# Kernel optimization log

Measured on AMD Instinct MI355X. Metric: run time of the kernel, lower is better.

## Reference

```python
import jax, jax.numpy as jnp
import numpy as np

NUM_HEADS = 16  # matches init_kwargs


def _linear(x, W, b):
    # torch nn.Linear: x @ W.T + b
    return jnp.matmul(x, W.T) + b


def setup_inputs() -> dict:
    key = jax.random.key(0)
    ks = jax.random.split(key, 5)
    B, S, Dm = 8, 2048, 1024
    scale = 0.02
    return {
        "q": jax.random.normal(ks[0], (B, S, Dm), dtype=jnp.float32),
        "k": jax.random.normal(ks[1], (B, S, Dm), dtype=jnp.float32),
        "v": jax.random.normal(ks[2], (B, S, Dm), dtype=jnp.float32),
        "W": jax.random.normal(ks[3], (Dm, Dm), dtype=jnp.float32) * scale,
        "b": jax.random.normal(ks[4], (Dm,), dtype=jnp.float32) * scale,
    }


def reference(q, k, v, W, b):
    B, S, Dm = q.shape
    H = NUM_HEADS
    D = Dm // H  # head_dim

    def proj(x):
        # linear -> view(B, S, H, D) -> transpose(2, 3): (B, S, D, H)
        # NOTE: original code transposes dims 2 and 3 (head_dim <-> heads),
        # NOT the usual (1, 2); we reproduce that exactly.
        y = _linear(x, W, b).reshape(B, S, H, D)
        return jnp.swapaxes(y, 2, 3)  # (B, S, D, H)

    qh, kh, vh = proj(q), proj(k), proj(v)

    # scores: (B, S, D, H) @ (B, S, H, D) -> (B, S, D, D), scaled by sqrt(head_dim)
    logits = jnp.einsum("bsdh,bseh->bsde", qh, kh) / jnp.sqrt(jnp.float32(D))
    attn = jax.nn.softmax(logits, axis=-1)
    out = jnp.einsum("bsde,bseh->bsdh", attn, vh)  # (B, S, D, H)

    # transpose(1, 2) -> (B, D, S, H), then view(B, -1, model_dim)
    concat = jnp.swapaxes(out, 1, 2).reshape(B, -1, Dm)  # (B, S, Dm)
    return _linear(concat, W, b)
```

## Files before the change

### kernel.cpp

```cpp
#include <hip/hip_runtime.h>
#include <hip/hip_fp16.h>
#include <math.h>

typedef _Float16 f16;
typedef _Float16 half8_t __attribute__((ext_vector_type(8)));
typedef _Float16 half2_t __attribute__((ext_vector_type(2)));
typedef __fp16   fp16x2  __attribute__((ext_vector_type(2)));
typedef float    float4_t __attribute__((ext_vector_type(4)));

__device__ f16 Wh[1024 * 1024];

__device__ __forceinline__ void gl_lds16(const void* g, void* l) {
    __builtin_amdgcn_global_load_lds(
        (const __attribute__((address_space(1))) void*)g,
        (__attribute__((address_space(3))) void*)l,
        16, 0, 0);
}

__device__ __forceinline__ half2_t pkrtz(float a, float b) {
    fp16x2 r = __builtin_amdgcn_cvt_pkrtz(a, b);
    return __builtin_bit_cast(half2_t, r);
}

__device__ __forceinline__ float fdot2(half2_t a, half2_t b, float c) {
    return __builtin_amdgcn_fdot2(__builtin_bit_cast(fp16x2, a),
                                  __builtin_bit_cast(fp16x2, b), c, false);
}

__device__ __forceinline__ half8_t cvt8(float4_t lo, float4_t hi) {
    half2_t p0 = pkrtz(lo[0], lo[1]);
    half2_t p1 = pkrtz(lo[2], lo[3]);
    half2_t p2 = pkrtz(hi[0], hi[1]);
    half2_t p3 = pkrtz(hi[2], hi[3]);
    half8_t r;
    r[0] = p0[0]; r[1] = p0[1]; r[2] = p1[0]; r[3] = p1[1];
    r[4] = p2[0]; r[5] = p2[1]; r[6] = p3[0]; r[7] = p3[1];
    return r;
}

__global__ __launch_bounds__(256) void convert_w_kernel(const float* __restrict__ W) {
    const int i = (blockIdx.x * 256 + threadIdx.x) * 8;
    const float4_t a = *(const float4_t*)(W + i);
    const float4_t b = *(const float4_t*)(W + i + 4);
    half8_t h;
#pragma unroll
    for (int t = 0; t < 4; ++t) h[t] = (f16)a[t];
#pragma unroll
    for (int t = 0; t < 4; ++t) h[4 + t] = (f16)b[t];
    *(half8_t*)(Wh + i) = h;
}

template <typename TA, typename TC>
__device__ __forceinline__ void gemm_tile(
    const TA* __restrict__ A, const float* __restrict__ bias,
    TC* __restrict__ C)
{
    constexpr int K = 1024, N = 1024;
    constexpr bool AF32 = (sizeof(TA) == 4);
    __shared__ __align__(16) char smem[(AF32 ? 32768 : 16384) + 16384];
    float* Asf = (float*)smem;
    f16*   Ash = (f16*)smem;
    f16*   Bsh = (f16*)(smem + (AF32 ? 32768 : 16384));

    const int tid  = threadIdx.x;
    const int lane = tid & 63;
    const int wave = tid >> 6;
    const int wm = (wave >> 1) << 6;
    const int wn = (wave & 1) << 6;
    const int row0 = blockIdx.x * 128;
    const int col0 = blockIdx.y * 128;
    const int lrow = lane & 15;
    const int kq   = lane >> 4;

    float4_t acc[4][4];
#pragma unroll
    for (int i = 0; i < 4; ++i)
#pragma unroll
        for (int j = 0; j < 4; ++j)
            acc[i][j] = (float4_t){0.f, 0.f, 0.f, 0.f};

    for (int kt = 0; kt < K; kt += 64) {
#pragma unroll
        for (int it = 0; it < 4; ++it) {
            const int ch = tid + it * 256;
            const int r = ch >> 3, s = ch & 7;
            const f16* src = Wh + (size_t)(col0 + r) * K + kt + ((s ^ (r & 7)) << 3);
            gl_lds16(src, Bsh + ch * 8);
        }
        if constexpr (AF32) {
#pragma unroll
            for (int it = 0; it < 8; ++it) {
                const int ch = tid + it * 256;
                const int r = ch >> 4, s = ch & 15;
                const float* src = (const float*)A + (size_t)(row0 + r) * K + kt + ((s ^ (r & 15)) << 2);
                gl_lds16(src, Asf + ch * 4);
            }
        } else {
#pragma unroll
            for (int it = 0; it < 4; ++it) {
                const int ch = tid + it * 256;
                const int r = ch >> 3, s = ch & 7;
                const f16* src = (const f16*)A + (size_t)(row0 + r) * K + kt + ((s ^ (r & 7)) << 3);
                gl_lds16(src, Ash + ch * 8);
            }
        }
        __syncthreads();

#pragma unroll
        for (int ks = 0; ks < 2; ++ks) {
            half8_t af[4], bf[4];
#pragma unroll
            for (int i = 0; i < 4; ++i) {
                const int m = wm + i * 16 + lrow;
                if constexpr (AF32) {
                    const int c0 = ks * 8 + kq * 2;
                    const float4_t lo = *(const float4_t*)(Asf + m * 64 + ((c0 ^ (m & 15)) << 2));
                    const float4_t hi = *(const float4_t*)(Asf + m * 64 + (((c0 + 1) ^ (m & 15)) << 2));
                    af[i] = cvt8(lo, hi);
                } else {
                    af[i] = *(const half8_t*)(Ash + m * 64 + (((ks * 4 + kq) ^ (m & 7)) << 3));
                }
            }
#pragma unroll
            for (int j = 0; j < 4; ++j) {
                const int n = wn + j * 16 + lrow;
                bf[j] = *(const half8_t*)(Bsh + n * 64 + (((ks * 4 + kq) ^ (n & 7)) << 3));
            }
#pragma unroll
            for (int i = 0; i < 4; ++i)
#pragma unroll
                for (int j = 0; j < 4; ++j)
                    acc[i][j] = __builtin_amdgcn_mfma_f32_16x16x32_f16(af[i], bf[j], acc[i][j], 0, 0, 0);
        }
        __syncthreads();
    }

    const int ccol  = lane & 15;
    const int rbase = (lane >> 4) << 2;
#pragma unroll
    for (int j = 0; j < 4; ++j) {
        const int gcol = col0 + wn + j * 16 + ccol;
        const float bv = bias[gcol];
#pragma unroll
        for (int i = 0; i < 4; ++i) {
#pragma unroll
            for (int r = 0; r < 4; ++r) {
                const int grow = row0 + wm + i * 16 + rbase + r;
                C[(size_t)grow * N + gcol] = (TC)(acc[i][j][r] + bv);
            }
        }
    }
}

template <typename TA, typename TC>
__global__ __launch_bounds__(256) void gemm_kernel(
    const TA* __restrict__ A, const float* __restrict__ bias,
    TC* __restrict__ C)
{
    gemm_tile<TA, TC>(A, bias, C);
}

__global__ __launch_bounds__(256) void gemm_proj_kernel(
    const float* __restrict__ q, const float* __restrict__ k,
    const float* __restrict__ v, const float* __restrict__ bias,
    f16* __restrict__ cq, f16* __restrict__ ck, f16* __restrict__ cv)
{
    const int z = blockIdx.z;
    const float* A = (z == 0) ? q : (z == 1) ? k : v;
    f16*         C = (z == 0) ? cq : (z == 1) ? ck : cv;
    gemm_tile<float, f16>(A, bias, C);
}

__global__ __launch_bounds__(256) void attn_kernel(
    const f16* __restrict__ pq, const f16* __restrict__ pk,
    const f16* __restrict__ pv, f16* __restrict__ outp)
{
    __shared__ __align__(16) f16 Ks[4][64][24];
    __shared__ __align__(16) f16 Vs[4][16][72];
    const int lane = threadIdx.x & 63;
    const int wave = threadIdx.x >> 6;
    const int p = blockIdx.x * 4 + wave;
    const int b = p >> 11;
    const int s = p & 2047;
    const f16* qptr = pq + (size_t)p * 1024;
    const f16* kptr = pk + (size_t)p * 1024;
    const f16* vptr = pv + (size_t)p * 1024;

    {
        const int h  = lane >> 2;
        const int e0 = (lane & 3) << 4;
        const half8_t k0 = *(const half8_t*)(kptr + lane * 16);
        const half8_t k1 = *(const half8_t*)(kptr + lane * 16 + 8);
#pragma unroll
        for (int t = 0; t < 8; ++t) {
            Ks[wave][e0 + t][h]     = k0[t];
            Ks[wave][e0 + 8 + t][h] = k1[t];
        }
        const half8_t v0 = *(const half8_t*)(vptr + lane * 16);
        const half8_t v1 = *(const half8_t*)(vptr + lane * 16 + 8);
        *(half8_t*)&Vs[wave][h][e0]     = v0;
        *(half8_t*)&Vs[wave][h][e0 + 8] = v1;
    }
    half2_t qp2[8];
#pragma unroll
    for (int h2 = 0; h2 < 8; ++h2) {
        half2_t t;
        t[0] = qptr[(2 * h2) * 64 + lane];
        t[1] = qptr[(2 * h2 + 1) * 64 + lane];
        qp2[h2] = t;
    }
    __syncthreads();

    float a[64];
#pragma unroll
    for (int e = 0; e < 64; ++e) {
        const half8_t* kr = (const half8_t*)&Ks[wave][e][0];
        const half8_t ka = kr[0];
        const half8_t kb = kr[1];
        float acc = 0.f;
#pragma unroll
        for (int t = 0; t < 4; ++t) {
            half2_t k2a; k2a[0] = ka[2 * t]; k2a[1] = ka[2 * t + 1];
            half2_t k2b; k2b[0] = kb[2 * t]; k2b[1] = kb[2 * t + 1];
            acc = fdot2(qp2[t], k2a, acc);
            acc = fdot2(qp2[4 + t], k2b, acc);
        }
        a[e] = acc;
    }

    float m = a[0];
#pragma unroll
    for (int e = 1; e < 64; ++e) m = fmaxf(m, a[e]);
    float sum = 0.f;
#pragma unroll
    for (int e = 0; e < 64; ++e) {
        const float t = __expf((a[e] - m) * 0.125f);
        a[e] = t;
        sum += t;
    }
    const float inv = 1.f / sum;

    half2_t pk2[32];
#pragma unroll
    for (int e2 = 0; e2 < 32; ++e2)
        pk2[e2] = pkrtz(a[2 * e2], a[2 * e2 + 1]);

    float o[16];
#pragma unroll
    for (int h = 0; h < 16; ++h) {
        const half8_t* vr = (const half8_t*)&Vs[wave][h][0];
        float acc = 0.f;
#pragma unroll
        for (int q8 = 0; q8 < 8; ++q8) {
            const half8_t vv = vr[q8];
#pragma unroll
            for (int t = 0; t < 4; ++t) {
                half2_t v2; v2[0] = vv[2 * t]; v2[1] = vv[2 * t + 1];
                acc = fdot2(pk2[q8 * 4 + t], v2, acc);
            }
        }
        o[h] = acc;
    }

    half8_t o0, o1;
#pragma unroll
    for (int h = 0; h < 8; ++h) o0[h] = (f16)(o[h] * inv);
#pragma unroll
    for (int h = 0; h < 8; ++h) o1[h] = (f16)(o[8 + h] * inv);
    f16* dst = outp + ((size_t)(b * 64 + lane) * 2048 + s) * 16;
    *(half8_t*)dst       = o0;
    *(half8_t*)(dst + 8) = o1;
}

extern "C" void kernel_launch(void* const* d_in, const int* in_sizes, int n_in,
                              void* d_out, int out_size, void* d_ws, size_t ws_size,
                              hipStream_t stream)
{
    const float* q    = (const float*)d_in[0];
    const float* k    = (const float*)d_in[1];
    const float* v    = (const float*)d_in[2];
    const float* W    = (const float*)d_in[3];
    const float* bias = (const float*)d_in[4];
    float* out = (float*)d_out;

    const int M = 16384;
    const size_t elems = (size_t)M * 1024;

    f16* projq = (f16*)d_ws;
    f16* attn  = projq + elems;
    f16* projk = (f16*)d_out;
    f16* projv = projk + elems;

    convert_w_kernel<<<512, 256, 0, stream>>>(W);

    dim3 gridp(M / 128, 1024 / 128, 3);
    gemm_proj_kernel<<<gridp, 256, 0, stream>>>(q, k, v, bias, projq, projk, projv);
    attn_kernel<<<M / 4, 256, 0, stream>>>(projq, projk, projv, attn);
    dim3 grid(M / 128, 1024 / 128);
    gemm_kernel<f16, float><<<grid, 256, 0, stream>>>(attn, bias, out);
}
```

Baseline: 448.3 us.

## Use 256x256 double-buffered GEMM tiles with register-staged fp32 A conversion

```diff
diff --git a/kernel.cpp b/kernel.cpp
--- a/kernel.cpp
+++ b/kernel.cpp
@@ -50,102 +50,178 @@
     *(half8_t*)(Wh + i) = h;
 }
 
+
+__device__ __forceinline__ void stage16(const f16* __restrict__ base, f16* dst,
+                                        int tid, int kt) {
+#pragma unroll
+    for (int it = 0; it < 4; ++it) {
+        const int ch = tid + it * 512;
+        const int r = ch >> 3, s = ch & 7;
+        gl_lds16(base + (size_t)r * 1024 + kt + ((s ^ (r & 7)) << 3), dst + ch * 8);
+    }
+}
+
+__device__ __forceinline__ void loadA32(const float* __restrict__ base, int tid,
+                                        int kt, int itbase, float4_t g[4]) {
+#pragma unroll
+    for (int it = 0; it < 2; ++it) {
+        const int ch = tid + (itbase + it) * 512;
+        const int r = ch >> 3, s = ch & 7;
+        const float* p = base + (size_t)r * 1024 + kt + ((s ^ (r & 7)) << 3);
+        g[2 * it]     = *(const float4_t*)p;
+        g[2 * it + 1] = *(const float4_t*)(p + 4);
+    }
+}
+
+__device__ __forceinline__ void writeA32(f16* dst, int tid, int itbase,
+                                         const float4_t g[4]) {
+#pragma unroll
+    for (int it = 0; it < 2; ++it) {
+        const int ch = tid + (itbase + it) * 512;
+        *(half8_t*)(dst + ch * 8) = cvt8(g[2 * it], g[2 * it + 1]);
+    }
+}
+
 template <typename TA, typename TC>
-__device__ __forceinline__ void gemm_tile(
-    const TA* __restrict__ A, const float* __restrict__ bias,
-    TC* __restrict__ C)
-{
-    constexpr int K = 1024, N = 1024;
+__device__ __forceinline__ void gemm_tile256(const TA* __restrict__ A,
+                                             const float* __restrict__ bias,
+                                             TC* __restrict__ C) {
+    constexpr int K = 1024, N = 1024, NT = 16;
     constexpr bool AF32 = (sizeof(TA) == 4);
-    __shared__ __align__(16) char smem[(AF32 ? 32768 : 16384) + 16384];
-    float* Asf = (float*)smem;
-    f16*   Ash = (f16*)smem;
-    f16*   Bsh = (f16*)(smem + (AF32 ? 32768 : 16384));
+    __shared__ __align__(16) f16 smem[65536];
+    f16* const Asb = smem;
+    f16* const Bsb = smem + 32768;
 
     const int tid  = threadIdx.x;
     const int lane = tid & 63;
     const int wave = tid >> 6;
-    const int wm = (wave >> 1) << 6;
-    const int wn = (wave & 1) << 6;
-    const int row0 = blockIdx.x * 128;
-    const int col0 = blockIdx.y * 128;
+    const int wr   = wave >> 2;
+    const int wc   = wave & 3;
     const int lrow = lane & 15;
     const int kq   = lane >> 4;
-
-    float4_t acc[4][4];
-#pragma unroll
-    for (int i = 0; i < 4; ++i)
+    const int row0 = blockIdx.x * 256;
+    const int col0 = blockIdx.y * 256;
+
+    const f16*   Ag16 = nullptr;
+    const float* Ag32 = nullptr;
+    if constexpr (AF32) Ag32 = (const float*)A + (size_t)row0 * K;
+    else                Ag16 = (const f16*)A + (size_t)row0 * K;
+    const f16* const Bg = Wh + (size_t)col0 * K;
+
+    float4_t acc[8][4];
+#pragma unroll
+    for (int i = 0; i < 8; ++i)
 #pragma unroll
         for (int j = 0; j < 4; ++j)
             acc[i][j] = (float4_t){0.f, 0.f, 0.f, 0.f};
 
-    for (int kt = 0; kt < K; kt += 64) {
-#pragma unroll
-        for (int it = 0; it < 4; ++it) {
-            const int ch = tid + it * 256;
-            const int r = ch >> 3, s = ch & 7;
-            const f16* src = Wh + (size_t)(col0 + r) * K + kt + ((s ^ (r & 7)) << 3);
-            gl_lds16(src, Bsh + ch * 8);
-        }
+    if constexpr (AF32) {
+        stage16(Bg, Bsb, tid, 0);
+        float4_t g0[4], g1[4];
+        loadA32(Ag32, tid, 0, 0, g0);
+        loadA32(Ag32, tid, 0, 2, g1);
+        writeA32(Asb, tid, 0, g0);
+        writeA32(Asb, tid, 2, g1);
+        asm volatile("s_waitcnt vmcnt(0)" ::: "memory");
+        asm volatile("s_waitcnt lgkmcnt(0)" ::: "memory");
+    } else {
+        stage16(Ag16, Asb, tid, 0);
+        stage16(Bg, Bsb, tid, 0);
+    }
+
+    for (int u = 0; u < NT; ++u) {
+        const int cur = u & 1;
+        const f16* const Ac = Asb + (cur << 14);
+        const f16* const Bc = Bsb + (cur << 14);
+        f16* const An = Asb + ((cur ^ 1) << 14);
+        f16* const Bn = Bsb + ((cur ^ 1) << 14);
+        const int kn = ((u + 1) & (NT - 1)) * 64;
+
+        float4_t ga[4];
+        stage16(Bg, Bn, tid, kn);
         if constexpr (AF32) {
-#pragma unroll
-            for (int it = 0; it < 8; ++it) {
-                const int ch = tid + it * 256;
-                const int r = ch >> 4, s = ch & 15;
-                const float* src = (const float*)A + (size_t)(row0 + r) * K + kt + ((s ^ (r & 15)) << 2);
-                gl_lds16(src, Asf + ch * 4);
+            loadA32(Ag32, tid, kn, 0, ga);
+        } else {
+            stage16(Ag16, An, tid, kn);
+        }
+        asm volatile("s_waitcnt vmcnt(8)" ::: "memory");
+        __builtin_amdgcn_s_barrier();
+
+        half8_t bfv[4][2];
+#pragma unroll
+        for (int j = 0; j < 4; ++j) {
+            const int n = wc * 64 + j * 16 + lrow;
+#pragma unroll
+            for (int ks = 0; ks < 2; ++ks)
+                bfv[j][ks] = *(const half8_t*)(Bc + n * 64 + (((ks * 4 + kq) ^ (n & 7)) << 3));
+        }
+
+        {
+            half8_t afv[4][2];
+#pragma unroll
+            for (int i = 0; i < 4; ++i) {
+                const int m = wr * 128 + i * 16 + lrow;
+#pragma unroll
+                for (int ks = 0; ks < 2; ++ks)
+                    afv[i][ks] = *(const half8_t*)(Ac + m * 64 + (((ks * 4 + kq) ^ (m & 7)) << 3));
             }
-        } else {
-#pragma unroll
-            for (int it = 0; it < 4; ++it) {
-                const int ch = tid + it * 256;
-                const int r = ch >> 3, s = ch & 7;
-                const f16* src = (const f16*)A + (size_t)(row0 + r) * K + kt + ((s ^ (r & 7)) << 3);
-                gl_lds16(src, Ash + ch * 8);
+            __builtin_amdgcn_s_setprio(1);
+#pragma unroll
+            for (int i = 0; i < 4; ++i)
+#pragma unroll
+                for (int j = 0; j < 4; ++j)
+#pragma unroll
+                    for (int ks = 0; ks < 2; ++ks)
+                        acc[i][j] = __builtin_amdgcn_mfma_f32_16x16x32_f16(
+                            afv[i][ks], bfv[j][ks], acc[i][j], 0, 0, 0);
+            __builtin_amdgcn_s_setprio(0);
+        }
+
+        if constexpr (AF32) {
+            writeA32(An, tid, 0, ga);
+            loadA32(Ag32, tid, kn, 2, ga);
+        }
+
+        {
+            half8_t afv[4][2];
+#pragma unroll
+            for (int i = 0; i < 4; ++i) {
+                const int m = wr * 128 + (4 + i) * 16 + lrow;
+#pragma unroll
+                for (int ks = 0; ks < 2; ++ks)
+                    afv[i][ks] = *(const half8_t*)(Ac + m * 64 + (((ks * 4 + kq) ^ (m & 7)) << 3));
             }
-        }
-        __syncthreads();
-
-#pragma unroll
-        for (int ks = 0; ks < 2; ++ks) {
-            half8_t af[4], bf[4];
-#pragma unroll
-            for (int i = 0; i < 4; ++i) {
-                const int m = wm + i * 16 + lrow;
-                if constexpr (AF32) {
-                    const int c0 = ks * 8 + kq * 2;
-                    const float4_t lo = *(const float4_t*)(Asf + m * 64 + ((c0 ^ (m & 15)) << 2));
-                    const float4_t hi = *(const float4_t*)(Asf + m * 64 + (((c0 + 1) ^ (m & 15)) << 2));
-                    af[i] = cvt8(lo, hi);
-                } else {
-                    af[i] = *(const half8_t*)(Ash + m * 64 + (((ks * 4 + kq) ^ (m & 7)) << 3));
-                }
-            }
-#pragma unroll
-            for (int j = 0; j < 4; ++j) {
-                const int n = wn + j * 16 + lrow;
-                bf[j] = *(const half8_t*)(Bsh + n * 64 + (((ks * 4 + kq) ^ (n & 7)) << 3));
-            }
+            __builtin_amdgcn_s_setprio(1);
 #pragma unroll
             for (int i = 0; i < 4; ++i)
 #pragma unroll
                 for (int j = 0; j < 4; ++j)
-                    acc[i][j] = __builtin_amdgcn_mfma_f32_16x16x32_f16(af[i], bf[j], acc[i][j], 0, 0, 0);
-        }
-        __syncthreads();
-    }
+#pragma unroll
+                    for (int ks = 0; ks < 2; ++ks)
+                        acc[4 + i][j] = __builtin_amdgcn_mfma_f32_16x16x32_f16(
+                            afv[i][ks], bfv[j][ks], acc[4 + i][j], 0, 0, 0);
+            __builtin_amdgcn_s_setprio(0);
+        }
+
+        if constexpr (AF32) {
+            writeA32(An, tid, 2, ga);
+        }
+        asm volatile("s_waitcnt lgkmcnt(0)" ::: "memory");
+        __builtin_amdgcn_s_barrier();
+    }
+    asm volatile("s_waitcnt vmcnt(0)" ::: "memory");
 
     const int ccol  = lane & 15;
     const int rbase = (lane >> 4) << 2;
 #pragma unroll
     for (int j = 0; j < 4; ++j) {
-        const int gcol = col0 + wn + j * 16 + ccol;
+        const int gcol = col0 + wc * 64 + j * 16 + ccol;
         const float bv = bias[gcol];
 #pragma unroll
-        for (int i = 0; i < 4; ++i) {
+        for (int i = 0; i < 8; ++i) {
 #pragma unroll
             for (int r = 0; r < 4; ++r) {
-                const int grow = row0 + wm + i * 16 + rbase + r;
+                const int grow = row0 + wr * 128 + i * 16 + rbase + r;
                 C[(size_t)grow * N + gcol] = (TC)(acc[i][j][r] + bv);
             }
         }
@@ -153,22 +229,20 @@
 }
 
 template <typename TA, typename TC>
-__global__ __launch_bounds__(256) void gemm_kernel(
+__global__ __launch_bounds__(512, 2) void gemm_kernel(
     const TA* __restrict__ A, const float* __restrict__ bias,
-    TC* __restrict__ C)
-{
-    gemm_tile<TA, TC>(A, bias, C);
-}
-
-__global__ __launch_bounds__(256) void gemm_proj_kernel(
+    TC* __restrict__ C) {
+    gemm_tile256<TA, TC>(A, bias, C);
+}
+
+__global__ __launch_bounds__(512, 2) void gemm_proj_kernel(
     const float* __restrict__ q, const float* __restrict__ k,
     const float* __restrict__ v, const float* __restrict__ bias,
-    f16* __restrict__ cq, f16* __restrict__ ck, f16* __restrict__ cv)
-{
+    f16* __restrict__ cq, f16* __restrict__ ck, f16* __restrict__ cv) {
     const int z = blockIdx.z;
     const float* A = (z == 0) ? q : (z == 1) ? k : v;
     f16*         C = (z == 0) ? cq : (z == 1) ? ck : cv;
-    gemm_tile<float, f16>(A, bias, C);
+    gemm_tile256<float, f16>(A, bias, C);
 }
 
 __global__ __launch_bounds__(256) void attn_kernel(
@@ -293,9 +367,9 @@
 
     convert_w_kernel<<<512, 256, 0, stream>>>(W);
 
-    dim3 gridp(M / 128, 1024 / 128, 3);
-    gemm_proj_kernel<<<gridp, 256, 0, stream>>>(q, k, v, bias, projq, projk, projv);
+    dim3 gridp(M / 256, 1024 / 256, 3);
+    gemm_proj_kernel<<<gridp, 512, 0, stream>>>(q, k, v, bias, projq, projk, projv);
     attn_kernel<<<M / 4, 256, 0, stream>>>(projq, projk, projv, attn);
-    dim3 grid(M / 128, 1024 / 128);
-    gemm_kernel<f16, float><<<grid, 256, 0, stream>>>(attn, bias, out);
-}
+    dim3 gridf(M / 256, 1024 / 256);
+    gemm_kernel<f16, float><<<gridf, 512, 0, stream>>>(attn, bias, out);
+}
```

Result: faster. 427.1 us (-4.7%).
